# Kernel tuning notes

Measured on AMD Instinct MI355X. Metric: run time of the kernel, lower is better.

The kernel has to match this reference:

```python
import jax, jax.numpy as jnp
import numpy as np

N_WORDS, N_BOOKS, L_WORD = 64, 128, 32
TAU_Q = 10.0
EPS = 1e-12  # matches torch F.normalize eps clamp


def setup_inputs() -> dict:
    key = jax.random.key(0)
    kx, kc = jax.random.split(key)
    x = jax.random.normal(kx, (16384, N_BOOKS * L_WORD), dtype=jnp.float32)
    # xavier_normal_(gain=0.1) on [64, 4096]: std = 0.1*sqrt(2/(64+4096))
    std = 0.1 * np.sqrt(2.0 / (N_WORDS + N_BOOKS * L_WORD))
    C = jax.random.normal(kc, (N_WORDS, N_BOOKS * L_WORD), dtype=jnp.float32) * std
    return {"x": x, "C": C}


def reference(x, C):
    N = x.shape[0]
    xb = x.reshape(N, N_BOOKS, L_WORD)          # [N, B, L]
    cb = C.reshape(N_WORDS, N_BOOKS, L_WORD)    # [W, B, L]
    # per-book L2 normalization of codewords (feature_normlization on C)
    cnorm = jnp.sqrt(jnp.sum(cb * cb, axis=-1, keepdims=True))
    cb = cb / jnp.maximum(cnorm, EPS)
    x2 = jnp.sum(xb * xb, axis=-1)[:, :, None]          # [N, B, 1]
    c2 = jnp.sum(cb * cb, axis=-1).T[None, :, :]        # [1, B, W]
    xc = jnp.einsum('nbl,wbl->nbw', xb, cb)             # [N, B, W]
    dist = x2 + c2 - 2.0 * xc
    soft = jax.nn.softmax(-TAU_Q * dist, axis=-1)       # [N, B, W]
    Z = jnp.einsum('nbw,wbl->nbl', soft, cb).reshape(N, N_BOOKS * L_WORD)
    idx = jnp.argmin(dist, axis=-1)                     # [N, B]
    return Z, idx
```

## Files before the change

kernel.cpp:

```cpp
#include <hip/hip_runtime.h>
#include <math.h>

#define NROWS   16384
#define NBOOKS  128
#define NWORDS  64
#define LWORD   32
#define DIMS    4096
#define T2K     28.8539008177792681472f
#define Z_ELEMS 67108864ull

typedef __attribute__((ext_vector_type(8))) short s16x8;
typedef __attribute__((ext_vector_type(4))) float f32x4;
typedef __attribute__((ext_vector_type(4))) unsigned int u32x4;

#define CBT_OFF  0u
#define C2T_OFF  1048576u
#define FR_OFF   1114112u
#define CTR_OFF  3211264u
#define LIST_OFF 3211392u
#define LIST_CAP 131072u

__device__ __forceinline__ unsigned short f2bf(float f) {
    unsigned int u = __float_as_uint(f);
    unsigned int r = (u + 0x7FFFu + ((u >> 16) & 1u)) >> 16;
    return (unsigned short)r;
}
__device__ __forceinline__ float bf2f(unsigned short s) {
    return __uint_as_float(((unsigned int)s) << 16);
}
__device__ __forceinline__ unsigned int cvtpk_bf16(float lo, float hi) {
    unsigned int r;
    asm("v_cvt_pk_bf16_f32 %0, %1, %2" : "=v"(r) : "v"(lo), "v"(hi));
    return r;
}

__device__ __forceinline__ float np_sum32(const float* a) {
#pragma clang fp contract(off)
    float r0 = a[0], r1 = a[1], r2 = a[2], r3 = a[3];
    float r4 = a[4], r5 = a[5], r6 = a[6], r7 = a[7];
    r0 += a[8];  r1 += a[9];  r2 += a[10]; r3 += a[11];
    r4 += a[12]; r5 += a[13]; r6 += a[14]; r7 += a[15];
    r0 += a[16]; r1 += a[17]; r2 += a[18]; r3 += a[19];
    r4 += a[20]; r5 += a[21]; r6 += a[22]; r7 += a[23];
    r0 += a[24]; r1 += a[25]; r2 += a[26]; r3 += a[27];
    r4 += a[28]; r5 += a[29]; r6 += a[30]; r7 += a[31];
    return ((r0 + r1) + (r2 + r3)) + ((r4 + r5) + (r6 + r7));
}

__global__ __launch_bounds__(64) void prepC_kernel(const float* __restrict__ C,
                                                   float* __restrict__ cbT,
                                                   float* __restrict__ c2T,
                                                   s16x8* __restrict__ fr,
                                                   unsigned int* __restrict__ ctr) {
    __shared__ float cb_s[NWORDS][33];
    __shared__ float c2_s[NWORDS];
    int b = blockIdx.x;
    int w = threadIdx.x;
    if (b == 0 && w == 0) ctr[0] = 0u;

    float cb[LWORD];
    float c2;
    {
#pragma clang fp contract(off)
        const float* src = C + (size_t)w * DIMS + b * LWORD;
        float v[LWORD];
        #pragma unroll
        for (int q = 0; q < 8; ++q)
            *(float4*)&v[4 * q] = *(const float4*)&src[4 * q];
        float sq[LWORD];
        #pragma unroll
        for (int l = 0; l < LWORD; ++l) sq[l] = v[l] * v[l];
        float nrm = fmaxf(sqrtf(np_sum32(sq)), 1e-12f);
        #pragma unroll
        for (int l = 0; l < LWORD; ++l) cb[l] = v[l] / nrm;
        float sq2[LWORD];
        #pragma unroll
        for (int l = 0; l < LWORD; ++l) sq2[l] = cb[l] * cb[l];
        c2 = np_sum32(sq2);
    }
    float* dst = cbT + ((size_t)b * NWORDS + w) * LWORD;
    #pragma unroll
    for (int q = 0; q < 8; ++q)
        *(float4*)&dst[4 * q] = *(const float4*)&cb[4 * q];
    c2T[b * NWORDS + w] = c2;
    #pragma unroll
    for (int l = 0; l < LWORD; ++l) cb_s[w][l] = cb[l];
    c2_s[w] = c2;
    __syncthreads();

    int lr = w & 15, lh = w >> 4;
    #pragma unroll
    for (int wb = 0; wb < 4; ++wb) {
        s16x8 ch8, cl8, a28;
        #pragma unroll
        for (int i = 0; i < 8; ++i) {
            float f = cb_s[wb * 16 + lr][lh * 8 + i];
            unsigned short hh = f2bf(f);
            ch8[i] = (short)hh;
            cl8[i] = (short)f2bf(f - bf2f(hh));
            a28[i] = (short)f2bf(cb_s[(wb & 1) * 32 + lh * 8 + i][(wb >> 1) * 16 + lr]);
        }
        f32x4 civ = {-0.5f * c2_s[wb * 16 + lh * 4 + 0],
                     -0.5f * c2_s[wb * 16 + lh * 4 + 1],
                     -0.5f * c2_s[wb * 16 + lh * 4 + 2],
                     -0.5f * c2_s[wb * 16 + lh * 4 + 3]};
        s16x8* d = fr + ((size_t)(b * 4 + wb) * 64 + w) * 4;
        d[0] = ch8;
        d[1] = cl8;
        d[2] = a28;
        d[3] = __builtin_bit_cast(s16x8, civ);
    }
}

#define GROUP_TAIL(ACC, G)                                                             \
  {                                                                                    \
    float q0 = fmaxf(fmaxf(ACC[0][0], ACC[0][1]), ACC[0][2]);                          \
    float q1 = fmaxf(fmaxf(ACC[0][3], ACC[1][0]), ACC[1][1]);                          \
    float q2 = fmaxf(fmaxf(ACC[1][2], ACC[1][3]), ACC[2][0]);                          \
    float q3 = fmaxf(fmaxf(ACC[2][1], ACC[2][2]), ACC[2][3]);                          \
    float q4 = fmaxf(fmaxf(ACC[3][0], ACC[3][1]), ACC[3][2]);                          \
    float m1 = fmaxf(fmaxf(fmaxf(q0, q1), q2), fmaxf(fmaxf(q3, q4), ACC[3][3]));       \
    m1 = fmaxf(m1, __shfl_xor(m1, 16));                                                \
    m1 = fmaxf(m1, __shfl_xor(m1, 32));                                                \
    float thr = m1 - 2e-4f;                                                            \
    int cnt = 0;                                                                       \
    _Pragma("unroll")                                                                  \
    for (int wb = 0; wb < 4; ++wb)                                                     \
      _Pragma("unroll")                                                                \
      for (int r = 0; r < 4; ++r) cnt += (ACC[wb][r] > thr) ? 1 : 0;                   \
    cnt += __shfl_xor(cnt, 16);                                                        \
    cnt += __shfl_xor(cnt, 32);                                                        \
    int wsel = 9999;                                                                   \
    _Pragma("unroll")                                                                  \
    for (int wb = 0; wb < 4; ++wb)                                                     \
      _Pragma("unroll")                                                                \
      for (int r = 0; r < 4; ++r)                                                      \
        if (ACC[wb][r] == m1) wsel = min(wsel, wb * 16 + h * 4 + r);                   \
    wsel = min(wsel, __shfl_xor(wsel, 16));                                            \
    wsel = min(wsel, __shfl_xor(wsel, 32));                                            \
    float mqt = m1 * (-T2K);                                                           \
    float p[16];                                                                       \
    float sum = 0.f;                                                                   \
    _Pragma("unroll")                                                                  \
    for (int wb = 0; wb < 4; ++wb)                                                     \
      _Pragma("unroll")                                                                \
      for (int r = 0; r < 4; ++r) {                                                    \
        p[wb * 4 + r] = __builtin_amdgcn_exp2f(fmaf(T2K, ACC[wb][r], mqt));            \
        sum += p[wb * 4 + r];                                                          \
      }                                                                                \
    sum += __shfl_xor(sum, 16);                                                        \
    sum += __shfl_xor(sum, 32);                                                        \
    float inv = __builtin_amdgcn_rcpf(sum);                                            \
    unsigned int pku[8];                                                               \
    _Pragma("unroll")                                                                  \
    for (int k = 0; k < 8; ++k) pku[k] = cvtpk_bf16(p[2 * k], p[2 * k + 1]);           \
    _Pragma("unroll")                                                                  \
    for (int wb = 0; wb < 4; ++wb) {                                                   \
      uint2 w2; w2.x = pku[2 * wb]; w2.y = pku[2 * wb + 1];                            \
      *(uint2*)&ps_s[wid][(G) & 1][c][wb * 16 + h * 4] = w2;                           \
    }                                                                                  \
    s16x8 pb0 = *(const s16x8*)&ps_s[wid][(G) & 1][c][h * 8];                          \
    s16x8 pb1 = *(const s16x8*)&ps_s[wid][(G) & 1][c][32 + h * 8];                     \
    float* zout = zbase + (size_t)(G) * 16 * DIMS;                                     \
    _Pragma("unroll")                                                                  \
    for (int mb = 0; mb < 2; ++mb) {                                                   \
      f32x4 z = {0.f, 0.f, 0.f, 0.f};                                                  \
      z = __builtin_amdgcn_mfma_f32_16x16x32_bf16(a2f[mb * 2 + 0], pb0, z, 0, 0, 0);   \
      z = __builtin_amdgcn_mfma_f32_16x16x32_bf16(a2f[mb * 2 + 1], pb1, z, 0, 0, 0);   \
      float4 v;                                                                        \
      v.x = z[0] * inv; v.y = z[1] * inv; v.z = z[2] * inv; v.w = z[3] * inv;          \
      *(float4*)(zout + mb * 16) = v;                                                  \
    }                                                                                  \
    if (h == 0) {                                                                      \
      int row = n0 + wid * 64 + (G) * 16 + c;                                          \
      out[Z_ELEMS + (size_t)row * NBOOKS + b] = (float)wsel;                           \
      if (cnt >= 2) {                                                                  \
        unsigned int pos = atomicAdd(ctr, 1u);                                         \
        if (pos < LIST_CAP) list[pos] = ((unsigned int)row << 7) | (unsigned int)b;    \
      }                                                                                \
    }                                                                                  \
  }

__global__ __launch_bounds__(256, 3) void softpq_mfma(const float* __restrict__ x,
                                                      const s16x8* __restrict__ fr,
                                                      unsigned int* __restrict__ ctr,
                                                      unsigned int* __restrict__ list,
                                                      float* __restrict__ out) {
    __shared__ __align__(16) unsigned short ps_s[4][2][16][72];

    int u = blockIdx.x;
    int L = (u & 7) * 1024 + (u >> 3);
    int b  = L >> 6;
    int n0 = (L & 63) * 256;
    int t  = threadIdx.x;
    int lane = t & 63, wid = t >> 6;
    int h = lane >> 4, c = lane & 15;

    const float* xbase = x + (size_t)(n0 + wid * 64 + c) * DIMS + b * LWORD + h * 8;
    float4 xa[4], xb[4];
    #pragma unroll
    for (int g = 0; g < 4; ++g) {
        xa[g] = *(const float4*)(xbase + (size_t)g * 16 * DIMS);
        xb[g] = *(const float4*)(xbase + (size_t)g * 16 * DIMS + 4);
    }

    const s16x8* fp = fr + ((size_t)b * 4 * 64 + lane) * 4;
    s16x8 chf[4], clf[4], a2f[4];
    f32x4 ci[4];
    #pragma unroll
    for (int wb = 0; wb < 4; ++wb) {
        const s16x8* q = fp + (size_t)wb * 256;
        chf[wb] = q[0];
        clf[wb] = q[1];
        a2f[wb] = q[2];
        ci[wb]  = __builtin_bit_cast(f32x4, q[3]);
    }

    unsigned int xh[4][4], xl[4][4];
    #pragma unroll
    for (int g = 0; g < 4; ++g) {
        float xf[8] = {xa[g].x, xa[g].y, xa[g].z, xa[g].w,
                       xb[g].x, xb[g].y, xb[g].z, xb[g].w};
        #pragma unroll
        for (int j = 0; j < 4; ++j) {
            float f0 = xf[2 * j], f1 = xf[2 * j + 1];
            unsigned int ph = cvtpk_bf16(f0, f1);
            float h0 = __uint_as_float(ph << 16);
            float h1 = __uint_as_float(ph & 0xffff0000u);
            xh[g][j] = ph;
            xl[g][j] = cvtpk_bf16(f0 - h0, f1 - h1);
        }
    }

    float* zbase = out + (size_t)(n0 + wid * 64 + c) * DIMS + b * LWORD + h * 4;

    #pragma unroll
    for (int gp = 0; gp < 2; ++gp) {
        int g0 = gp * 2, g1 = gp * 2 + 1;
        u32x4 th0 = {xh[g0][0], xh[g0][1], xh[g0][2], xh[g0][3]};
        u32x4 tl0 = {xl[g0][0], xl[g0][1], xl[g0][2], xl[g0][3]};
        u32x4 th1 = {xh[g1][0], xh[g1][1], xh[g1][2], xh[g1][3]};
        u32x4 tl1 = {xl[g1][0], xl[g1][1], xl[g1][2], xl[g1][3]};
        s16x8 xh0 = __builtin_bit_cast(s16x8, th0);
        s16x8 xl0 = __builtin_bit_cast(s16x8, tl0);
        s16x8 xh1 = __builtin_bit_cast(s16x8, th1);
        s16x8 xl1 = __builtin_bit_cast(s16x8, tl1);

        __builtin_amdgcn_s_setprio(1);
        f32x4 acc0[4], acc1[4];
        #pragma unroll
        for (int wb = 0; wb < 4; ++wb) {
            f32x4 a = ci[wb];
            a = __builtin_amdgcn_mfma_f32_16x16x32_bf16(chf[wb], xh0, a, 0, 0, 0);
            a = __builtin_amdgcn_mfma_f32_16x16x32_bf16(chf[wb], xl0, a, 0, 0, 0);
            a = __builtin_amdgcn_mfma_f32_16x16x32_bf16(clf[wb], xh0, a, 0, 0, 0);
            acc0[wb] = a;
        }
        #pragma unroll
        for (int wb = 0; wb < 4; ++wb) {
            f32x4 a = ci[wb];
            a = __builtin_amdgcn_mfma_f32_16x16x32_bf16(chf[wb], xh1, a, 0, 0, 0);
            a = __builtin_amdgcn_mfma_f32_16x16x32_bf16(chf[wb], xl1, a, 0, 0, 0);
            a = __builtin_amdgcn_mfma_f32_16x16x32_bf16(clf[wb], xh1, a, 0, 0, 0);
            acc1[wb] = a;
        }
        __builtin_amdgcn_s_setprio(0);

        GROUP_TAIL(acc0, g0)
        GROUP_TAIL(acc1, g1)
    }
}

__global__ __launch_bounds__(256) void rescan_wave(const float* __restrict__ x,
                                                   const float* __restrict__ cbT,
                                                   const float* __restrict__ c2T,
                                                   const unsigned int* __restrict__ ctr,
                                                   const unsigned int* __restrict__ list,
                                                   float* __restrict__ out) {
    unsigned int n = *ctr;
    if (n > LIST_CAP) n = LIST_CAP;
    unsigned int wgl = blockIdx.x * 4u + (threadIdx.x >> 6);
    unsigned int nw  = gridDim.x * 4u;
    int lane = threadIdx.x & 63;

    for (unsigned int i = wgl; i < n; i += nw) {
        unsigned int e = list[i];
        int row = (int)(e >> 7);
        int b   = (int)(e & 127u);

        const float* xrow = x + (size_t)row * DIMS + b * LWORD;
        float xr2[LWORD];
        #pragma unroll
        for (int q = 0; q < 8; ++q)
            *(float4*)&xr2[q * 4] = *(const float4*)(xrow + q * 4);
        float sq[LWORD];
        #pragma unroll
        for (int l = 0; l < LWORD; ++l) sq[l] = xr2[l] * xr2[l];
        float x2n = np_sum32(sq);

        const float* cw = cbT + ((size_t)b * NWORDS + lane) * LWORD;
        float cwv[LWORD];
        #pragma unroll
        for (int q = 0; q < 8; ++q)
            *(float4*)&cwv[q * 4] = *(const float4*)(cw + q * 4);
        double a0 = 0.0, a1 = 0.0, a2 = 0.0, a3 = 0.0;
        #pragma unroll
        for (int l = 0; l < 8; ++l) {
            a0 = fma((double)xr2[l],      (double)cwv[l],      a0);
            a1 = fma((double)xr2[l + 8],  (double)cwv[l + 8],  a1);
            a2 = fma((double)xr2[l + 16], (double)cwv[l + 16], a2);
            a3 = fma((double)xr2[l + 24], (double)cwv[l + 24], a3);
        }
        float xcf = (float)((a0 + a1) + (a2 + a3));
        float dnp;
        {
#pragma clang fp contract(off)
            float s1 = x2n + c2T[b * NWORDS + lane];
            float s2 = 2.0f * xcf;
            dnp = s1 - s2;
        }
        float dmin = dnp;
        dmin = fminf(dmin, __shfl_xor(dmin, 1));
        dmin = fminf(dmin, __shfl_xor(dmin, 2));
        dmin = fminf(dmin, __shfl_xor(dmin, 4));
        dmin = fminf(dmin, __shfl_xor(dmin, 8));
        dmin = fminf(dmin, __shfl_xor(dmin, 16));
        dmin = fminf(dmin, __shfl_xor(dmin, 32));
        unsigned long long ball = __ballot(dnp == dmin);
        int wbest = __ffsll((long long)ball) - 1;
        if (lane == 0)
            out[Z_ELEMS + (size_t)row * NBOOKS + b] = (float)wbest;
    }
}

extern "C" void kernel_launch(void* const* d_in, const int* in_sizes, int n_in,
                              void* d_out, int out_size, void* d_ws, size_t ws_size,
                              hipStream_t stream) {
    const float* x = (const float*)d_in[0];
    const float* C = (const float*)d_in[1];
    float* out = (float*)d_out;
    char* ws = (char*)d_ws;
    float* cbT = (float*)(ws + CBT_OFF);
    float* c2T = (float*)(ws + C2T_OFF);
    s16x8* fr  = (s16x8*)(ws + FR_OFF);
    unsigned int* ctr  = (unsigned int*)(ws + CTR_OFF);
    unsigned int* list = (unsigned int*)(ws + LIST_OFF);

    prepC_kernel<<<128, 64, 0, stream>>>(C, cbT, c2T, fr, ctr);
    softpq_mfma<<<8192, 256, 0, stream>>>(x, fr, ctr, list, out);
    rescan_wave<<<512, 256, 0, stream>>>(x, cbT, c2T, ctr, list, out);
}
```

Baseline: 160.7 us.

## Stage codeword fragments in LDS and use 512-thread blocks with fewer rows per wave

The main kernel now uses 8 waves per block, with each wave handling 2 row-groups instead of 4. Codebook fragments are loaded once per block into shared memory instead of being held in registers by every wave. The fragment layout written by prepC is changed to suit a coalesced block-wide copy. The aim is to cut register pressure and raise occupancy, so more waves can hide the memory latency of the streaming x loads and Z stores. The cost is an extra __syncthreads, LDS reads inside the MFMA loops, and less work per wave to amortise setup.

```diff
diff --git a/kernel.cpp b/kernel.cpp
--- a/kernel.cpp
+++ b/kernel.cpp
@@ -89,6 +89,7 @@
     __syncthreads();
 
     int lr = w & 15, lh = w >> 4;
+    s16x8* frb = fr + (size_t)b * 1024;
     #pragma unroll
     for (int wb = 0; wb < 4; ++wb) {
         s16x8 ch8, cl8, a28;
@@ -104,15 +105,14 @@
                      -0.5f * c2_s[wb * 16 + lh * 4 + 1],
                      -0.5f * c2_s[wb * 16 + lh * 4 + 2],
                      -0.5f * c2_s[wb * 16 + lh * 4 + 3]};
-        s16x8* d = fr + ((size_t)(b * 4 + wb) * 64 + w) * 4;
-        d[0] = ch8;
-        d[1] = cl8;
-        d[2] = a28;
-        d[3] = __builtin_bit_cast(s16x8, civ);
-    }
-}
-
-#define GROUP_TAIL(ACC, G)                                                             \
+        frb[(wb * 4 + 0) * 64 + w] = ch8;
+        frb[(wb * 4 + 1) * 64 + w] = cl8;
+        frb[(wb * 4 + 2) * 64 + w] = a28;
+        frb[(wb * 4 + 3) * 64 + w] = __builtin_bit_cast(s16x8, civ);
+    }
+}
+
+#define GROUP_TAIL(ACC, G, ROW)                                                        \
   {                                                                                    \
     float q0 = fmaxf(fmaxf(ACC[0][0], ACC[0][1]), ACC[0][2]);                          \
     float q1 = fmaxf(fmaxf(ACC[0][3], ACC[1][0]), ACC[1][1]);                          \
@@ -157,36 +157,38 @@
     _Pragma("unroll")                                                                  \
     for (int wb = 0; wb < 4; ++wb) {                                                   \
       uint2 w2; w2.x = pku[2 * wb]; w2.y = pku[2 * wb + 1];                            \
-      *(uint2*)&ps_s[wid][(G) & 1][c][wb * 16 + h * 4] = w2;                           \
+      *(uint2*)&ps_s[wid][G][c][wb * 16 + h * 4] = w2;                                 \
     }                                                                                  \
-    s16x8 pb0 = *(const s16x8*)&ps_s[wid][(G) & 1][c][h * 8];                          \
-    s16x8 pb1 = *(const s16x8*)&ps_s[wid][(G) & 1][c][32 + h * 8];                     \
-    float* zout = zbase + (size_t)(G) * 16 * DIMS;                                     \
+    s16x8 pb0 = *(const s16x8*)&ps_s[wid][G][c][h * 8];                                \
+    s16x8 pb1 = *(const s16x8*)&ps_s[wid][G][c][32 + h * 8];                           \
+    float* zout = out + (size_t)(ROW) * DIMS + b * LWORD + h * 4;                      \
     _Pragma("unroll")                                                                  \
     for (int mb = 0; mb < 2; ++mb) {                                                   \
+      s16x8 a20 = frag_s[((mb * 2 + 0) * 4 + 2) * 64 + lane];                          \
+      s16x8 a21 = frag_s[((mb * 2 + 1) * 4 + 2) * 64 + lane];                          \
       f32x4 z = {0.f, 0.f, 0.f, 0.f};                                                  \
-      z = __builtin_amdgcn_mfma_f32_16x16x32_bf16(a2f[mb * 2 + 0], pb0, z, 0, 0, 0);   \
-      z = __builtin_amdgcn_mfma_f32_16x16x32_bf16(a2f[mb * 2 + 1], pb1, z, 0, 0, 0);   \
+      z = __builtin_amdgcn_mfma_f32_16x16x32_bf16(a20, pb0, z, 0, 0, 0);               \
+      z = __builtin_amdgcn_mfma_f32_16x16x32_bf16(a21, pb1, z, 0, 0, 0);               \
       float4 v;                                                                        \
       v.x = z[0] * inv; v.y = z[1] * inv; v.z = z[2] * inv; v.w = z[3] * inv;          \
       *(float4*)(zout + mb * 16) = v;                                                  \
     }                                                                                  \
     if (h == 0) {                                                                      \
-      int row = n0 + wid * 64 + (G) * 16 + c;                                          \
-      out[Z_ELEMS + (size_t)row * NBOOKS + b] = (float)wsel;                           \
+      out[Z_ELEMS + (size_t)(ROW) * NBOOKS + b] = (float)wsel;                         \
       if (cnt >= 2) {                                                                  \
         unsigned int pos = atomicAdd(ctr, 1u);                                         \
-        if (pos < LIST_CAP) list[pos] = ((unsigned int)row << 7) | (unsigned int)b;    \
+        if (pos < LIST_CAP) list[pos] = ((unsigned int)(ROW) << 7) | (unsigned int)b;  \
       }                                                                                \
     }                                                                                  \
   }
 
-__global__ __launch_bounds__(256, 3) void softpq_mfma(const float* __restrict__ x,
+__global__ __launch_bounds__(512, 6) void softpq_mfma(const float* __restrict__ x,
                                                       const s16x8* __restrict__ fr,
                                                       unsigned int* __restrict__ ctr,
                                                       unsigned int* __restrict__ list,
                                                       float* __restrict__ out) {
-    __shared__ __align__(16) unsigned short ps_s[4][2][16][72];
+    __shared__ __align__(16) s16x8 frag_s[1024];
+    __shared__ __align__(16) unsigned short ps_s[8][2][16][72];
 
     int u = blockIdx.x;
     int L = (u & 7) * 1024 + (u >> 3);
@@ -195,80 +197,83 @@
     int t  = threadIdx.x;
     int lane = t & 63, wid = t >> 6;
     int h = lane >> 4, c = lane & 15;
-
-    const float* xbase = x + (size_t)(n0 + wid * 64 + c) * DIMS + b * LWORD + h * 8;
-    float4 xa[4], xb[4];
-    #pragma unroll
-    for (int g = 0; g < 4; ++g) {
-        xa[g] = *(const float4*)(xbase + (size_t)g * 16 * DIMS);
-        xb[g] = *(const float4*)(xbase + (size_t)g * 16 * DIMS + 4);
-    }
-
-    const s16x8* fp = fr + ((size_t)b * 4 * 64 + lane) * 4;
-    s16x8 chf[4], clf[4], a2f[4];
-    f32x4 ci[4];
-    #pragma unroll
-    for (int wb = 0; wb < 4; ++wb) {
-        const s16x8* q = fp + (size_t)wb * 256;
-        chf[wb] = q[0];
-        clf[wb] = q[1];
-        a2f[wb] = q[2];
-        ci[wb]  = __builtin_bit_cast(f32x4, q[3]);
-    }
-
-    unsigned int xh[4][4], xl[4][4];
-    #pragma unroll
-    for (int g = 0; g < 4; ++g) {
-        float xf[8] = {xa[g].x, xa[g].y, xa[g].z, xa[g].w,
-                       xb[g].x, xb[g].y, xb[g].z, xb[g].w};
+    int row0 = n0 + wid * 16 + c;
+    int row1 = row0 + 128;
+
+    const float* xp0 = x + (size_t)row0 * DIMS + b * LWORD + h * 8;
+    const float* xp1 = x + (size_t)row1 * DIMS + b * LWORD + h * 8;
+    float4 xa0 = *(const float4*)xp0;
+    float4 xb0 = *(const float4*)(xp0 + 4);
+    float4 xa1 = *(const float4*)xp1;
+    float4 xb1 = *(const float4*)(xp1 + 4);
+
+    {
+        const s16x8* g = fr + (size_t)b * 1024 + t * 2;
+        s16x8 g0 = g[0];
+        s16x8 g1 = g[1];
+        frag_s[t * 2]     = g0;
+        frag_s[t * 2 + 1] = g1;
+    }
+    __syncthreads();
+
+    s16x8 xhv0, xlv0, xhv1, xlv1;
+    {
+        float xf[8] = {xa0.x, xa0.y, xa0.z, xa0.w, xb0.x, xb0.y, xb0.z, xb0.w};
+        unsigned int xhu[4], xlu[4];
         #pragma unroll
         for (int j = 0; j < 4; ++j) {
             float f0 = xf[2 * j], f1 = xf[2 * j + 1];
             unsigned int ph = cvtpk_bf16(f0, f1);
             float h0 = __uint_as_float(ph << 16);
             float h1 = __uint_as_float(ph & 0xffff0000u);
-            xh[g][j] = ph;
-            xl[g][j] = cvtpk_bf16(f0 - h0, f1 - h1);
-        }
-    }
-
-    float* zbase = out + (size_t)(n0 + wid * 64 + c) * DIMS + b * LWORD + h * 4;
-
+            xhu[j] = ph;
+            xlu[j] = cvtpk_bf16(f0 - h0, f1 - h1);
+        }
+        u32x4 thv = {xhu[0], xhu[1], xhu[2], xhu[3]};
+        u32x4 tlv = {xlu[0], xlu[1], xlu[2], xlu[3]};
+        xhv0 = __builtin_bit_cast(s16x8, thv);
+        xlv0 = __builtin_bit_cast(s16x8, tlv);
+    }
+    {
+        float xf[8] = {xa1.x, xa1.y, xa1.z, xa1.w, xb1.x, xb1.y, xb1.z, xb1.w};
+        unsigned int xhu[4], xlu[4];
+        #pragma unroll
+        for (int j = 0; j < 4; ++j) {
+            float f0 = xf[2 * j], f1 = xf[2 * j + 1];
+            unsigned int ph = cvtpk_bf16(f0, f1);
+            float h0 = __uint_as_float(ph << 16);
+            float h1 = __uint_as_float(ph & 0xffff0000u);
+            xhu[j] = ph;
+            xlu[j] = cvtpk_bf16(f0 - h0, f1 - h1);
+        }
+        u32x4 thv = {xhu[0], xhu[1], xhu[2], xhu[3]};
+        u32x4 tlv = {xlu[0], xlu[1], xlu[2], xlu[3]};
+        xhv1 = __builtin_bit_cast(s16x8, thv);
+        xlv1 = __builtin_bit_cast(s16x8, tlv);
+    }
+
+    f32x4 acc0[4], acc1[4];
+    __builtin_amdgcn_s_setprio(1);
     #pragma unroll
-    for (int gp = 0; gp < 2; ++gp) {
-        int g0 = gp * 2, g1 = gp * 2 + 1;
-        u32x4 th0 = {xh[g0][0], xh[g0][1], xh[g0][2], xh[g0][3]};
-        u32x4 tl0 = {xl[g0][0], xl[g0][1], xl[g0][2], xl[g0][3]};
-        u32x4 th1 = {xh[g1][0], xh[g1][1], xh[g1][2], xh[g1][3]};
-        u32x4 tl1 = {xl[g1][0], xl[g1][1], xl[g1][2], xl[g1][3]};
-        s16x8 xh0 = __builtin_bit_cast(s16x8, th0);
-        s16x8 xl0 = __builtin_bit_cast(s16x8, tl0);
-        s16x8 xh1 = __builtin_bit_cast(s16x8, th1);
-        s16x8 xl1 = __builtin_bit_cast(s16x8, tl1);
-
-        __builtin_amdgcn_s_setprio(1);
-        f32x4 acc0[4], acc1[4];
-        #pragma unroll
-        for (int wb = 0; wb < 4; ++wb) {
-            f32x4 a = ci[wb];
-            a = __builtin_amdgcn_mfma_f32_16x16x32_bf16(chf[wb], xh0, a, 0, 0, 0);
-            a = __builtin_amdgcn_mfma_f32_16x16x32_bf16(chf[wb], xl0, a, 0, 0, 0);
-            a = __builtin_amdgcn_mfma_f32_16x16x32_bf16(clf[wb], xh0, a, 0, 0, 0);
-            acc0[wb] = a;
-        }
-        #pragma unroll
-        for (int wb = 0; wb < 4; ++wb) {
-            f32x4 a = ci[wb];
-            a = __builtin_amdgcn_mfma_f32_16x16x32_bf16(chf[wb], xh1, a, 0, 0, 0);
-            a = __builtin_amdgcn_mfma_f32_16x16x32_bf16(chf[wb], xl1, a, 0, 0, 0);
-            a = __builtin_amdgcn_mfma_f32_16x16x32_bf16(clf[wb], xh1, a, 0, 0, 0);
-            acc1[wb] = a;
-        }
-        __builtin_amdgcn_s_setprio(0);
-
-        GROUP_TAIL(acc0, g0)
-        GROUP_TAIL(acc1, g1)
-    }
+    for (int wb = 0; wb < 4; ++wb) {
+        s16x8 chf = frag_s[(wb * 4 + 0) * 64 + lane];
+        s16x8 clf = frag_s[(wb * 4 + 1) * 64 + lane];
+        f32x4 ci  = __builtin_bit_cast(f32x4, frag_s[(wb * 4 + 3) * 64 + lane]);
+        f32x4 a0 = ci;
+        a0 = __builtin_amdgcn_mfma_f32_16x16x32_bf16(chf, xhv0, a0, 0, 0, 0);
+        a0 = __builtin_amdgcn_mfma_f32_16x16x32_bf16(chf, xlv0, a0, 0, 0, 0);
+        a0 = __builtin_amdgcn_mfma_f32_16x16x32_bf16(clf, xhv0, a0, 0, 0, 0);
+        acc0[wb] = a0;
+        f32x4 a1 = ci;
+        a1 = __builtin_amdgcn_mfma_f32_16x16x32_bf16(chf, xhv1, a1, 0, 0, 0);
+        a1 = __builtin_amdgcn_mfma_f32_16x16x32_bf16(chf, xlv1, a1, 0, 0, 0);
+        a1 = __builtin_amdgcn_mfma_f32_16x16x32_bf16(clf, xhv1, a1, 0, 0, 0);
+        acc1[wb] = a1;
+    }
+    __builtin_amdgcn_s_setprio(0);
+
+    GROUP_TAIL(acc0, 0, row0)
+    GROUP_TAIL(acc1, 1, row1)
 }
 
 __global__ __launch_bounds__(256) void rescan_wave(const float* __restrict__ x,
@@ -347,6 +352,6 @@
     unsigned int* list = (unsigned int*)(ws + LIST_OFF);
 
     prepC_kernel<<<128, 64, 0, stream>>>(C, cbT, c2T, fr, ctr);
-    softpq_mfma<<<8192, 256, 0, stream>>>(x, fr, ctr, list, out);
+    softpq_mfma<<<8192, 512, 0, stream>>>(x, fr, ctr, list, out);
     rescan_wave<<<512, 256, 0, stream>>>(x, cbT, c2T, ctr, list, out);
 }
```

Result: faster. 154.9 us (median of 2 runs) (-3.6%).
